# Optimization experiments

Hardware: AMD Instinct MI355X
Metric: run time of the kernel (lower is better)

Reference implementation:

```python
import jax, jax.numpy as jnp
import numpy as np
from jax import lax

TOL = 1e-06
POSINF = 1000000.0
NEGINF = -1000000.0


def _grad1(x, axis):
    """torch.gradient with spacing=1, edge_order=1 along `axis`:
    central differences in the interior, one-sided at the edges."""
    n = x.shape[axis]
    left = lax.slice_in_dim(x, 0, n - 2, axis=axis)
    right = lax.slice_in_dim(x, 2, n, axis=axis)
    interior = (right - left) * 0.5
    first = lax.slice_in_dim(x, 1, 2, axis=axis) - lax.slice_in_dim(x, 0, 1, axis=axis)
    last = lax.slice_in_dim(x, n - 1, n, axis=axis) - lax.slice_in_dim(x, n - 2, n - 1, axis=axis)
    return jnp.concatenate([first, interior, last], axis=axis)


def _clean(g):
    g = jnp.nan_to_num(g, nan=0.0, posinf=POSINF, neginf=NEGINF)
    return jnp.where(jnp.abs(g) < TOL, jnp.zeros_like(g), g)


def setup_inputs() -> dict:
    key = jax.random.key(0)
    k1, k2 = jax.random.split(key)
    shape = (8, 4, 64, 128, 128)  # [B, C=4, D, H, W]
    return {
        "input": jax.random.normal(k1, shape, dtype=jnp.float32),
        "target": jax.random.normal(k2, shape, dtype=jnp.float32),
    }


def reference(input, target):
    # spacing is ones per batch, so per-batch/per-channel loops collapse into
    # one vectorized finite-difference per spatial axis (dims 2, 3, 4).
    x = input.astype(jnp.float32)
    t = target.astype(jnp.float32)
    total = jnp.float32(0.0)
    for axis in (2, 3, 4):
        diff = _clean(_grad1(x, axis)) - _clean(_grad1(t, axis))
        # per-channel MSE (mean over b,d,h,w), then summed over the 4 channels
        total = total + jnp.sum(jnp.mean(diff * diff, axis=(0, 2, 3, 4)))
    return total
```

## Files before the change

### kernel.cpp

```cpp
#include <hip/hip_runtime.h>
#include <math.h>


#define Bn 8
#define Cn 4
#define Dn 64
#define Hn 128
#define Wn 128

static constexpr int HCHUNK = 8;
static constexpr int NTHREADS = 256;
static constexpr int NBLOCKS = 4096;
static constexpr int ROW = Wn / 4;
static constexpr int PLANE = Hn * ROW;

__global__ __launch_bounds__(NTHREADS) void gradloss_main(
        const float* __restrict__ xf, const float* __restrict__ tf,
        double* __restrict__ partials) {
    const int tid  = threadIdx.x;
    const int w4   = tid & 31;
    const int dlow = tid >> 5;
    const int b    = blockIdx.x;
    const int bc    = b & 31;
    const int hc    = (b >> 5) & 15;
    const int dhigh = b >> 9;
    const int d  = dhigh * 8 + dlow;
    const int h0 = hc * HCHUNK;

    const int base = ((bc * Dn + d) * Hn + h0) * ROW + w4;
    const float4* __restrict__ Xr = (const float4*)xf + base;
    const float4* __restrict__ Tr = (const float4*)tf + base;

    const int dpo = (d < Dn - 1) ? PLANE : 0;
    const int dmo = (d > 0) ? -PLANE : 0;
    const float sd2  = (d == 0 || d == Dn - 1) ? 1.0f : 0.25f;
    const float sw02 = (w4 == 0) ? 1.0f : 0.25f;
    const float sw32 = (w4 == 31) ? 1.0f : 0.25f;

    float4 uc, um;
    {
        const float4 xc = Xr[0], tc = Tr[0];
        uc.x = xc.x - tc.x; uc.y = xc.y - tc.y;
        uc.z = xc.z - tc.z; uc.w = xc.w - tc.w;
    }
    if (h0 > 0) {
        const float4 xm = Xr[-ROW], tm = Tr[-ROW];
        um.x = xm.x - tm.x; um.y = xm.y - tm.y;
        um.z = xm.z - tm.z; um.w = xm.w - tm.w;
    } else {
        um = uc;
    }

    float acc0 = 0.0f, acc1 = 0.0f, acc2 = 0.0f;
    #pragma unroll
    for (int hl = 0; hl < HCHUNK; ++hl) {
        const int h = h0 + hl;
        const int po = (h < Hn - 1) ? ROW : 0;
        const float4 xp  = Xr[po],  tp  = Tr[po];
        const float4 xdp = Xr[dpo], tdp = Tr[dpo];
        const float4 xdm = Xr[dmo], tdm = Tr[dmo];
        const float sh2 = (h == 0 || h == Hn - 1) ? 1.0f : 0.25f;

        float4 up;
        up.x = xp.x - tp.x; up.y = xp.y - tp.y;
        up.z = xp.z - tp.z; up.w = xp.w - tp.w;

        { const float dx = up.x - um.x; acc0 = fmaf(dx * dx, sh2, acc0); }
        { const float dx = up.y - um.y; acc0 = fmaf(dx * dx, sh2, acc0); }
        { const float dx = up.z - um.z; acc0 = fmaf(dx * dx, sh2, acc0); }
        { const float dx = up.w - um.w; acc0 = fmaf(dx * dx, sh2, acc0); }

        { const float dx = (xdp.x - xdm.x) - (tdp.x - tdm.x); acc1 = fmaf(dx * dx, sd2, acc1); }
        { const float dx = (xdp.y - xdm.y) - (tdp.y - tdm.y); acc1 = fmaf(dx * dx, sd2, acc1); }
        { const float dx = (xdp.z - xdm.z) - (tdp.z - tdm.z); acc1 = fmaf(dx * dx, sd2, acc1); }
        { const float dx = (xdp.w - xdm.w) - (tdp.w - tdm.w); acc1 = fmaf(dx * dx, sd2, acc1); }

        const float ulw = __shfl_up(uc.w, 1, 32);
        const float urx = __shfl_down(uc.x, 1, 32);
        const float ul = (w4 == 0)  ? uc.x : ulw;
        const float ur = (w4 == 31) ? uc.w : urx;
        { const float dx = uc.y - ul;   acc2 = fmaf(dx * dx, sw02, acc2); }
        { const float dx = uc.z - uc.x; acc2 = fmaf(dx * dx, 0.25f, acc2); }
        { const float dx = uc.w - uc.y; acc2 = fmaf(dx * dx, 0.25f, acc2); }
        { const float dx = ur - uc.z;   acc2 = fmaf(dx * dx, sw32, acc2); }

        um = uc; uc = up;
        Xr += ROW; Tr += ROW;
    }

    float acc = (acc0 + acc1) + acc2;

    for (int off = 32; off > 0; off >>= 1)
        acc += __shfl_down(acc, off, 64);

    __shared__ float wsum[NTHREADS / 64];
    const int lane = tid & 63;
    const int wid = tid >> 6;
    if (lane == 0) wsum[wid] = acc;
    __syncthreads();
    if (tid == 0) {
        double bsum = (double)wsum[0] + (double)wsum[1] +
                      (double)wsum[2] + (double)wsum[3];
        partials[blockIdx.x] = bsum;
    }
}

__global__ __launch_bounds__(256) void gradloss_reduce(
        const double* __restrict__ partials, float* __restrict__ out, int n) {
    double a = 0.0;
    for (int i = threadIdx.x; i < n; i += 256) a += partials[i];
    for (int off = 32; off > 0; off >>= 1)
        a += __shfl_down(a, off, 64);
    __shared__ double s[4];
    const int lane = threadIdx.x & 63;
    const int wid = threadIdx.x >> 6;
    if (lane == 0) s[wid] = a;
    __syncthreads();
    if (threadIdx.x == 0) {
        double tot = s[0] + s[1] + s[2] + s[3];
        out[0] = (float)(tot / 8388608.0);
    }
}

extern "C" void kernel_launch(void* const* d_in, const int* in_sizes, int n_in,
                              void* d_out, int out_size, void* d_ws, size_t ws_size,
                              hipStream_t stream) {
    const float* x = (const float*)d_in[0];
    const float* t = (const float*)d_in[1];
    float* out = (float*)d_out;
    double* partials = (double*)d_ws;

    gradloss_main<<<NBLOCKS, NTHREADS, 0, stream>>>(x, t, partials);
    gradloss_reduce<<<1, 256, 0, stream>>>(partials, out, NBLOCKS);
}
```

Measured before the change: 290.1 us.

## Share depth neighbours through LDS instead of reloading from global memory

Each thread now writes its input-minus-target row into a double-buffered shared-memory tile. Edge threads (dlow 0 and 7) also load one halo plane each, and the depth gradient reads its neighbours from LDS rather than doing four extra global loads per row per thread. This removes the threefold read amplification on the depth axis, at the cost of a __syncthreads per row and some LDS traffic. Launch bounds also now request higher occupancy.

```diff
diff --git a/kernel.cpp b/kernel.cpp
--- a/kernel.cpp
+++ b/kernel.cpp
@@ -14,7 +14,14 @@
 static constexpr int ROW = Wn / 4;
 static constexpr int PLANE = Hn * ROW;
 
-__global__ __launch_bounds__(NTHREADS) void gradloss_main(
+__device__ __forceinline__ float4 sub4(const float4 a, const float4 b) {
+    float4 r;
+    r.x = a.x - b.x; r.y = a.y - b.y;
+    r.z = a.z - b.z; r.w = a.w - b.w;
+    return r;
+}
+
+__global__ __launch_bounds__(NTHREADS, 8) void gradloss_main(
         const float* __restrict__ xf, const float* __restrict__ tf,
         double* __restrict__ partials) {
     const int tid  = threadIdx.x;
@@ -31,49 +38,48 @@
     const float4* __restrict__ Xr = (const float4*)xf + base;
     const float4* __restrict__ Tr = (const float4*)tf + base;
 
-    const int dpo = (d < Dn - 1) ? PLANE : 0;
-    const int dmo = (d > 0) ? -PLANE : 0;
+    const bool haloLow  = (dlow == 0);
+    const bool haloHigh = (dlow == 7);
+    const bool isHalo   = haloLow | haloHigh;
+    const int hoff = haloLow ? ((dhigh > 0) ? -PLANE : 0)
+                             : ((dhigh < 7) ?  PLANE : 0);
+
     const float sd2  = (d == 0 || d == Dn - 1) ? 1.0f : 0.25f;
     const float sw02 = (w4 == 0) ? 1.0f : 0.25f;
     const float sw32 = (w4 == 31) ? 1.0f : 0.25f;
 
-    float4 uc, um;
-    {
-        const float4 xc = Xr[0], tc = Tr[0];
-        uc.x = xc.x - tc.x; uc.y = xc.y - tc.y;
-        uc.z = xc.z - tc.z; uc.w = xc.w - tc.w;
-    }
-    if (h0 > 0) {
-        const float4 xm = Xr[-ROW], tm = Tr[-ROW];
-        um.x = xm.x - tm.x; um.y = xm.y - tm.y;
-        um.z = xm.z - tm.z; um.w = xm.w - tm.w;
-    } else {
-        um = uc;
-    }
+    __shared__ float4 uL[2][10][32];
+
+    float4 uc = sub4(Xr[0], Tr[0]);
+    float4 um;
+    if (h0 > 0) um = sub4(Xr[-ROW], Tr[-ROW]);
+    else        um = uc;
+    float4 hu;
+    if (isHalo) hu = sub4(Xr[hoff], Tr[hoff]);
+    else        hu = make_float4(0.f, 0.f, 0.f, 0.f);
 
     float acc0 = 0.0f, acc1 = 0.0f, acc2 = 0.0f;
+    int s = 0;
     #pragma unroll
     for (int hl = 0; hl < HCHUNK; ++hl) {
         const int h = h0 + hl;
         const int po = (h < Hn - 1) ? ROW : 0;
-        const float4 xp  = Xr[po],  tp  = Tr[po];
-        const float4 xdp = Xr[dpo], tdp = Tr[dpo];
-        const float4 xdm = Xr[dmo], tdm = Tr[dmo];
-        const float sh2 = (h == 0 || h == Hn - 1) ? 1.0f : 0.25f;
 
-        float4 up;
-        up.x = xp.x - tp.x; up.y = xp.y - tp.y;
-        up.z = xp.z - tp.z; up.w = xp.w - tp.w;
+        const float4 xn = Xr[po], tn = Tr[po];
+        float4 xh, th;
+        if (isHalo) { xh = Xr[hoff + po]; th = Tr[hoff + po]; }
 
-        { const float dx = up.x - um.x; acc0 = fmaf(dx * dx, sh2, acc0); }
-        { const float dx = up.y - um.y; acc0 = fmaf(dx * dx, sh2, acc0); }
-        { const float dx = up.z - um.z; acc0 = fmaf(dx * dx, sh2, acc0); }
-        { const float dx = up.w - um.w; acc0 = fmaf(dx * dx, sh2, acc0); }
+        uL[s][dlow + 1][w4] = uc;
+        if (haloLow)  uL[s][0][w4] = hu;
+        if (haloHigh) uL[s][9][w4] = hu;
+        __syncthreads();
 
-        { const float dx = (xdp.x - xdm.x) - (tdp.x - tdm.x); acc1 = fmaf(dx * dx, sd2, acc1); }
-        { const float dx = (xdp.y - xdm.y) - (tdp.y - tdm.y); acc1 = fmaf(dx * dx, sd2, acc1); }
-        { const float dx = (xdp.z - xdm.z) - (tdp.z - tdm.z); acc1 = fmaf(dx * dx, sd2, acc1); }
-        { const float dx = (xdp.w - xdm.w) - (tdp.w - tdm.w); acc1 = fmaf(dx * dx, sd2, acc1); }
+        const float4 udp = uL[s][dlow + 2][w4];
+        const float4 udm = uL[s][dlow][w4];
+        { const float dx = udp.x - udm.x; acc1 = fmaf(dx * dx, sd2, acc1); }
+        { const float dx = udp.y - udm.y; acc1 = fmaf(dx * dx, sd2, acc1); }
+        { const float dx = udp.z - udm.z; acc1 = fmaf(dx * dx, sd2, acc1); }
+        { const float dx = udp.w - udm.w; acc1 = fmaf(dx * dx, sd2, acc1); }
 
         const float ulw = __shfl_up(uc.w, 1, 32);
         const float urx = __shfl_down(uc.x, 1, 32);
@@ -84,8 +90,17 @@
         { const float dx = uc.w - uc.y; acc2 = fmaf(dx * dx, 0.25f, acc2); }
         { const float dx = ur - uc.z;   acc2 = fmaf(dx * dx, sw32, acc2); }
 
-        um = uc; uc = up;
+        const float4 un = sub4(xn, tn);
+        const float sh2 = (h == 0 || h == Hn - 1) ? 1.0f : 0.25f;
+        { const float dx = un.x - um.x; acc0 = fmaf(dx * dx, sh2, acc0); }
+        { const float dx = un.y - um.y; acc0 = fmaf(dx * dx, sh2, acc0); }
+        { const float dx = un.z - um.z; acc0 = fmaf(dx * dx, sh2, acc0); }
+        { const float dx = un.w - um.w; acc0 = fmaf(dx * dx, sh2, acc0); }
+
+        um = uc; uc = un;
+        if (isHalo) hu = sub4(xh, th);
         Xr += ROW; Tr += ROW;
+        s ^= 1;
     }
 
     float acc = (acc0 + acc1) + acc2;
@@ -111,13 +126,13 @@
     for (int i = threadIdx.x; i < n; i += 256) a += partials[i];
     for (int off = 32; off > 0; off >>= 1)
         a += __shfl_down(a, off, 64);
-    __shared__ double s[4];
+    __shared__ double sh[4];
     const int lane = threadIdx.x & 63;
     const int wid = threadIdx.x >> 6;
-    if (lane == 0) s[wid] = a;
+    if (lane == 0) sh[wid] = a;
     __syncthreads();
     if (threadIdx.x == 0) {
-        double tot = s[0] + s[1] + s[2] + s[3];
+        double tot = sh[0] + sh[1] + sh[2] + sh[3];
         out[0] = (float)(tot / 8388608.0);
     }
 }
```

Result: slower. 337.3 us (+16.3%).
